# Performance work log

Measured on AMD Instinct MI355X. Metric: run time of the kernel, lower is better.

Reference implementation:

```python
import jax, jax.numpy as jnp
import numpy as np

DIM = 2048
D_INNER = 2048
B = 4
T = 4096
INIT_DECAY = 0.5


def setup_inputs() -> dict:
    key = jax.random.key(0)
    k1, k2, k3 = jax.random.split(key, 3)
    x = jax.random.normal(k1, (B, T, DIM), dtype=jnp.float32)
    h0 = jnp.zeros((B, D_INNER), dtype=jnp.float32)
    # xavier_uniform for Linear(dim -> d_inner) and Linear(d_inner -> dim)
    lim_in = float(np.sqrt(6.0 / (DIM + D_INNER)))
    W_in = jax.random.uniform(k2, (D_INNER, DIM), minval=-lim_in, maxval=lim_in, dtype=jnp.float32)
    lim_out = float(np.sqrt(6.0 / (D_INNER + DIM)))
    W_out = jax.random.uniform(k3, (DIM, D_INNER), minval=-lim_out, maxval=lim_out, dtype=jnp.float32)
    init_log = float(np.log(INIT_DECAY / (1.0 - INIT_DECAY)))  # logit(0.5) = 0
    log_d = jnp.full((D_INNER,), init_log, dtype=jnp.float32)
    b = jnp.zeros((D_INNER,), dtype=jnp.float32)
    return {"x": x, "h0": h0, "W_in": W_in, "W_out": W_out, "log_d": log_d, "b": b}


def reference(x, h0, W_in, W_out, log_d, b):
    # x: [B, T, dim]
    d = jax.nn.sigmoid(log_d)                       # [D] per-dim decay in (0,1)
    xp = jax.nn.silu(jnp.einsum('btd,ed->bte', x, W_in))  # [B, T, D_inner]
    xs = jnp.swapaxes(xp, 0, 1)                     # [T, B, D]

    def step(h_prev, xt):
        h_new = d * (xt + h_prev) + b               # diagonal-decay recurrence
        out = h_new * jax.nn.silu(h_new)            # self-gating
        return h_new, out

    h_final, outs = jax.lax.scan(step, h0, xs)      # outs: [T, B, D]
    cell_out = jnp.swapaxes(outs, 0, 1)             # [B, T, D]
    output = jnp.einsum('bte,de->btd', cell_out, W_out)  # [B, T, dim]
    return output, h_final
```

## Files before the change

### kernel.cpp

```cpp
#include <hip/hip_runtime.h>
#include <hip/hip_bf16.h>

#define DIMV 2048
#define DIV  2048
#define BV   4
#define TV   4096
#define MV   (BV * TV)
#define GK   2048
#define NCH  64
#define CH   64

typedef __bf16 bf16x8 __attribute__((ext_vector_type(8)));
typedef __bf16 bf16x4 __attribute__((ext_vector_type(4)));
typedef float  floatx4 __attribute__((ext_vector_type(4)));

__device__ __forceinline__ void gload_lds16(const void* g, void* l) {
    __builtin_amdgcn_global_load_lds((const __attribute__((address_space(1))) void*)g,
                                     (__attribute__((address_space(3))) void*)l,
                                     16, 0, 0);
}

__global__ __launch_bounds__(256) void cvt_all(const float4* __restrict__ x,
                                               const float4* __restrict__ wi,
                                               const float4* __restrict__ wo,
                                               ushort4* __restrict__ xb,
                                               ushort4* __restrict__ wib,
                                               ushort4* __restrict__ wob) {
    int i = blockIdx.x * 256 + threadIdx.x;
    const float4* src;
    ushort4* dst;
    int off;
    if (i < 8388608)       { src = x;  dst = xb;  off = 0; }
    else if (i < 9437184)  { src = wi; dst = wib; off = 8388608; }
    else                   { src = wo; dst = wob; off = 9437184; }
    float4 v = src[i - off];
    __hip_bfloat16 a = __float2bfloat16(v.x);
    __hip_bfloat16 b = __float2bfloat16(v.y);
    __hip_bfloat16 c = __float2bfloat16(v.z);
    __hip_bfloat16 d = __float2bfloat16(v.w);
    ushort4 o;
    o.x = *(unsigned short*)&a;
    o.y = *(unsigned short*)&b;
    o.z = *(unsigned short*)&c;
    o.w = *(unsigned short*)&d;
    dst[i - off] = o;
}

template <int EPI>
__global__ __launch_bounds__(512, 2) void gemm256_bt(const __hip_bfloat16* __restrict__ A,
                                                     const __hip_bfloat16* __restrict__ Bt,
                                                     float* __restrict__ Cf,
                                                     __hip_bfloat16* __restrict__ Cb) {
    __shared__ __align__(16) char AsB[65536];
    __shared__ __align__(16) char BsB[65536];

    const int tid  = threadIdx.x;
    const int lane = tid & 63;
    const int wave = tid >> 6;
    const int wmh  = wave >> 2;
    const int wnh  = (wave >> 1) & 1;
    const int wno  = wave & 1;
    const int lr   = lane & 15;
    const int lq   = lane >> 4;

    const int p   = blockIdx.y * gridDim.x + blockIdx.x;
    const int swz = (p & 7) * 64 + (p >> 3);
    const int m0  = (swz >> 3) * 256;
    const int n0  = (swz & 7) * 256;

    const int rdswz = lr * 128 + ((lq * 16) ^ ((lr & 7) << 4));
    const int rds[2] = { rdswz, rdswz ^ 64 };
    const char* aRd0 = AsB + wmh * 16384;
    const char* bRd0 = BsB + wnh * 16384 + wno * 8192;

    const int srow = tid >> 3;
    const int scol = ((tid & 7) ^ (srow & 7)) * 8;
    const __hip_bfloat16* aS_h0g0 = A  + (size_t)(m0 +   0 +  0 + srow) * GK + scol;
    const __hip_bfloat16* aS_h0g1 = A  + (size_t)(m0 +   0 + 64 + srow) * GK + scol;
    const __hip_bfloat16* aS_h1g0 = A  + (size_t)(m0 + 128 +  0 + srow) * GK + scol;
    const __hip_bfloat16* aS_h1g1 = A  + (size_t)(m0 + 128 + 64 + srow) * GK + scol;
    const __hip_bfloat16* bS_h0g0 = Bt + (size_t)(n0 +   0 +  0 + srow) * GK + scol;
    const __hip_bfloat16* bS_h0g1 = Bt + (size_t)(n0 +   0 + 64 + srow) * GK + scol;
    const __hip_bfloat16* bS_h1g0 = Bt + (size_t)(n0 + 128 +  0 + srow) * GK + scol;
    const __hip_bfloat16* bS_h1g1 = Bt + (size_t)(n0 + 128 + 64 + srow) * GK + scol;

#define BARR  asm volatile("s_barrier" ::: "memory")
#define WAITL do { asm volatile("s_waitcnt lgkmcnt(0)" ::: "memory");          \
                   __builtin_amdgcn_sched_barrier(0); } while (0)
#define VMW(N_) asm volatile("s_waitcnt vmcnt(" #N_ ")" ::: "memory")

#define STG(SRC_, DST_, T_) gload_lds16((SRC_) + (size_t)(T_) * 64, (DST_))
#define ST_AG0(T_, C_) do {                                                    \
    STG(aS_h0g0, AsB + (C_) * 32768 +     0 + tid * 16, T_);                   \
    STG(aS_h1g0, AsB + (C_) * 32768 + 16384 + tid * 16, T_); } while (0)
#define ST_AG1(T_, C_) do {                                                    \
    STG(aS_h0g1, AsB + (C_) * 32768 +  8192 + tid * 16, T_);                   \
    STG(aS_h1g1, AsB + (C_) * 32768 + 24576 + tid * 16, T_); } while (0)
#define ST_BG0(T_, C_) do {                                                    \
    STG(bS_h0g0, BsB + (C_) * 32768 +     0 + tid * 16, T_);                   \
    STG(bS_h1g0, BsB + (C_) * 32768 + 16384 + tid * 16, T_); } while (0)
#define ST_BG1(T_, C_) do {                                                    \
    STG(bS_h0g1, BsB + (C_) * 32768 +  8192 + tid * 16, T_);                   \
    STG(bS_h1g1, BsB + (C_) * 32768 + 24576 + tid * 16, T_); } while (0)

#define RDPH_A(DST_, MI0_, C_)                                                 \
    _Pragma("unroll") for (int mi_ = 0; mi_ < 4; ++mi_)                        \
      _Pragma("unroll") for (int s_ = 0; s_ < 2; ++s_)                         \
        DST_[mi_][s_] = *(const bf16x8*)(aRd0 + (C_) * 32768 +                 \
                                         ((MI0_) + mi_) * 2048 + rds[s_]);
#define RDPH_B(DST_, NI0_, C_)                                                 \
    _Pragma("unroll") for (int ni_ = 0; ni_ < 2; ++ni_)                        \
      _Pragma("unroll") for (int s_ = 0; s_ < 2; ++s_)                         \
        DST_[ni_][s_] = *(const bf16x8*)(bRd0 + (C_) * 32768 +                 \
                                         ((NI0_) + ni_) * 2048 + rds[s_]);

#define QUAD(MI0_, NI0_, AF_, BF_)                                             \
    __builtin_amdgcn_s_setprio(1);                                             \
    _Pragma("unroll") for (int mi_ = 0; mi_ < 4; ++mi_)                        \
      _Pragma("unroll") for (int ni_ = 0; ni_ < 2; ++ni_)                      \
        _Pragma("unroll") for (int s_ = 0; s_ < 2; ++s_)                       \
          acc[(MI0_) + mi_][(NI0_) + ni_] =                                    \
            __builtin_amdgcn_mfma_f32_16x16x32_bf16(                           \
              AF_[mi_][s_], BF_[ni_][s_],                                      \
              acc[(MI0_) + mi_][(NI0_) + ni_], 0, 0, 0);                       \
    __builtin_amdgcn_s_setprio(0);

#define KTILE(T_, C_, MODE_) do {                                              \
    bf16x8 a03[4][2], a47[4][2], b01[2][2], b23[2][2];                         \
                                                        \
    RDPH_A(a03, 0, C_);                                                        \
    RDPH_B(b01, 0, C_);                                                        \
    BARR; WAITL;                                                               \
    QUAD(0, 0, a03, b01);                                                      \
    BARR;                                                                      \
                                                        \
    RDPH_B(b23, 2, C_);                                                        \
    if ((MODE_) == 1) { ST_AG0((T_) + 2, C_); }                                \
    BARR; WAITL;                                                               \
    QUAD(0, 2, a03, b23);                                                      \
    BARR;                                                                      \
                                                        \
    RDPH_A(a47, 4, C_);                                                        \
    if ((MODE_) == 1) { ST_BG0((T_) + 2, C_); }                                \
    BARR; WAITL;                                                               \
    QUAD(4, 2, a47, b23);                                                      \
    BARR;                                                                      \
                                                        \
    if ((MODE_) == 1) { ST_AG1((T_) + 2, C_); ST_BG1((T_) + 2, C_); }          \
    BARR;                                                                      \
    QUAD(4, 0, a47, b01);                                                      \
    if ((MODE_) == 1) { VMW(8); }                                              \
    if ((MODE_) == 2) { VMW(0); }                                              \
    BARR;                                                                      \
} while (0)

    floatx4 acc[8][4];
#pragma unroll
    for (int i = 0; i < 8; ++i)
#pragma unroll
        for (int j = 0; j < 4; ++j) acc[i][j] = 0.f;

    ST_AG0(0, 0); ST_BG0(0, 0); ST_AG1(0, 0); ST_BG1(0, 0);
    ST_AG0(1, 1); ST_BG0(1, 1); ST_AG1(1, 1); ST_BG1(1, 1);
    VMW(8); BARR;

    for (int t2 = 0; t2 < 15; ++t2) {
        KTILE(2 * t2,     0, 1);
        KTILE(2 * t2 + 1, 1, 1);
    }
    KTILE(30, 0, 2);
    KTILE(31, 1, 0);

#undef KTILE
#undef QUAD
#undef RDPH_A
#undef RDPH_B
#undef ST_AG0
#undef ST_AG1
#undef ST_BG0
#undef ST_BG1
#undef STG
#undef VMW
#undef WAITL
#undef BARR

    const int wm = wmh * 128;
    const int wn = (wave & 3) * 64;
#pragma unroll
    for (int mi = 0; mi < 8; ++mi) {
#pragma unroll
        for (int r = 0; r < 4; ++r) {
            const int row = m0 + wm + mi * 16 + lq * 4 + r;
#pragma unroll
            for (int ni = 0; ni < 4; ++ni) {
                const int col = n0 + wn + ni * 16 + lr;
                float v = acc[mi][ni][r];
                if (EPI == 1) {
                    float s = v / (1.f + __expf(-v));
                    Cb[(size_t)row * DIV + col] = __float2bfloat16(s);
                } else {
                    Cf[(size_t)row * DIMV + col] = v;
                }
            }
        }
    }
}

__global__ __launch_bounds__(256) void scan_carry(const __hip_bfloat16* __restrict__ xp,
                                                  const float* __restrict__ logd,
                                                  const float* __restrict__ bias,
                                                  float* __restrict__ carry) {
    const int eg = blockIdx.x * 256 + threadIdx.x;
    const int e0 = eg * 4;
    const int c = blockIdx.y;
    const int b = blockIdx.z;
    const float4 ld = ((const float4*)logd)[eg];
    const float4 bb = ((const float4*)bias)[eg];
    float dv[4] = {1.f / (1.f + __expf(-ld.x)), 1.f / (1.f + __expf(-ld.y)),
                   1.f / (1.f + __expf(-ld.z)), 1.f / (1.f + __expf(-ld.w))};
    float bv[4] = {bb.x, bb.y, bb.z, bb.w};
    const __hip_bfloat16* p = xp + ((size_t)(b * TV + c * CH)) * DIV + e0;
    float h[4] = {0.f, 0.f, 0.f, 0.f};
#pragma unroll 8
    for (int i = 0; i < CH; ++i) {
        bf16x4 v = *(const bf16x4*)(p + (size_t)i * DIV);
#pragma unroll
        for (int j = 0; j < 4; ++j)
            h[j] = dv[j] * ((float)v[j] + h[j]) + bv[j];
    }
    float4 o = {h[0], h[1], h[2], h[3]};
    *(float4*)&carry[((size_t)b * NCH + c) * DIV + e0] = o;
}

__global__ __launch_bounds__(256) void scan_apply(const __hip_bfloat16* __restrict__ xp,
                                                  const float* __restrict__ logd,
                                                  const float* __restrict__ bias,
                                                  const float* __restrict__ h0,
                                                  const float* __restrict__ carry,
                                                  __hip_bfloat16* __restrict__ cell,
                                                  float* __restrict__ hfin) {
    const int eg = blockIdx.x * 256 + threadIdx.x;
    const int e0 = eg * 4;
    const int c = blockIdx.y;
    const int b = blockIdx.z;
    const float4 ld = ((const float4*)logd)[eg];
    const float4 bb = ((const float4*)bias)[eg];
    float dv[4] = {1.f / (1.f + __expf(-ld.x)), 1.f / (1.f + __expf(-ld.y)),
                   1.f / (1.f + __expf(-ld.z)), 1.f / (1.f + __expf(-ld.w))};
    float bv[4] = {bb.x, bb.y, bb.z, bb.w};
    float dCH[4];
#pragma unroll
    for (int j = 0; j < 4; ++j) dCH[j] = __powf(dv[j], (float)CH);

    float4 H4 = *(const float4*)&h0[(size_t)b * DIV + e0];
    float H[4] = {H4.x, H4.y, H4.z, H4.w};
    for (int j = 0; j < c; ++j) {
        float4 cr = *(const float4*)&carry[((size_t)b * NCH + j) * DIV + e0];
#pragma unroll
        for (int q = 0; q < 4; ++q) H[q] = dCH[q] * H[q] + ((const float*)&cr)[q];
    }

    const size_t base = ((size_t)(b * TV + c * CH)) * DIV + e0;
    float h[4] = {H[0], H[1], H[2], H[3]};
#pragma unroll 4
    for (int i = 0; i < CH; ++i) {
        bf16x4 v = *(const bf16x4*)(xp + base + (size_t)i * DIV);
        ushort4 o;
        unsigned short* op = (unsigned short*)&o;
#pragma unroll
        for (int j = 0; j < 4; ++j) {
            h[j] = dv[j] * ((float)v[j] + h[j]) + bv[j];
            float cv = h[j] * (h[j] / (1.f + __expf(-h[j])));
            __hip_bfloat16 cb = __float2bfloat16(cv);
            op[j] = *(unsigned short*)&cb;
        }
        *(ushort4*)(cell + base + (size_t)i * DIV) = o;
    }
    if (c == NCH - 1) {
        float4 o = {h[0], h[1], h[2], h[3]};
        *(float4*)&hfin[(size_t)b * DIV + e0] = o;
    }
}

extern "C" void kernel_launch(void* const* d_in, const int* in_sizes, int n_in,
                              void* d_out, int out_size, void* d_ws, size_t ws_size,
                              hipStream_t stream) {
    const float* x     = (const float*)d_in[0];
    const float* h0    = (const float*)d_in[1];
    const float* W_in  = (const float*)d_in[2];
    const float* W_out = (const float*)d_in[3];
    const float* log_d = (const float*)d_in[4];
    const float* bias  = (const float*)d_in[5];

    float* out  = (float*)d_out;
    float* hfin = out + (size_t)BV * TV * DIMV;

    char* ws = (char*)d_ws;
    __hip_bfloat16* xb    = (__hip_bfloat16*)ws;
    __hip_bfloat16* cellb = xb;
    __hip_bfloat16* wib   = (__hip_bfloat16*)(ws + 67108864);
    __hip_bfloat16* wob   = (__hip_bfloat16*)(ws + 67108864 + 8388608);
    __hip_bfloat16* xpb   = (__hip_bfloat16*)(ws + 67108864 + 16777216);
    float*          carry = (float*)(ws + 134217728 + 16777216);

    {
        int n4 = 10485760;
        cvt_all<<<n4 / 256, 256, 0, stream>>>((const float4*)x, (const float4*)W_in,
                                              (const float4*)W_out,
                                              (ushort4*)xb, (ushort4*)wib, (ushort4*)wob);
    }

    gemm256_bt<1><<<dim3(DIV / 256, MV / 256), 512, 0, stream>>>(xb, wib, nullptr, xpb);

    scan_carry<<<dim3(DIV / 1024, NCH, BV), 256, 0, stream>>>(xpb, log_d, bias, carry);
    scan_apply<<<dim3(DIV / 1024, NCH, BV), 256, 0, stream>>>(xpb, log_d, bias, h0, carry, cellb, hfin);

    gemm256_bt<0><<<dim3(DIMV / 256, MV / 256), 512, 0, stream>>>(cellb, wob, out, nullptr);
}
```

Baseline: 559.0 us.

## Prefetch next k-tile fragments across tiles and drop explicit LDS waits in GEMM

Restructures the GEMM k-tile loop so the A and B register fragments for the next k-tile are read from LDS during the current tile's last MFMA phases, double-buffering the b01 fragments across iterations. It removes the explicit lgkmcnt(0) waits and sched barriers, leaving the compiler to insert them, and reorders the global-to-LDS staging issues along with a new vmcnt wait point. This aims to hide LDS read latency behind MFMA work, at the cost of more live registers and tighter correctness reliance on the barrier and vmcnt placement.

Result: slower. 695.5 us (+24.4%).

```diff
diff --git a/kernel.cpp b/kernel.cpp
--- a/kernel.cpp
+++ b/kernel.cpp
@@ -85,8 +85,6 @@
     const __hip_bfloat16* bS_h1g1 = Bt + (size_t)(n0 + 128 + 64 + srow) * GK + scol;
 
 #define BARR  asm volatile("s_barrier" ::: "memory")
-#define WAITL do { asm volatile("s_waitcnt lgkmcnt(0)" ::: "memory");          \
-                   __builtin_amdgcn_sched_barrier(0); } while (0)
 #define VMW(N_) asm volatile("s_waitcnt vmcnt(" #N_ ")" ::: "memory")
 
 #define STG(SRC_, DST_, T_) gload_lds16((SRC_) + (size_t)(T_) * 64, (DST_))
@@ -125,32 +123,31 @@
               acc[(MI0_) + mi_][(NI0_) + ni_], 0, 0, 0);                       \
     __builtin_amdgcn_s_setprio(0);
 
-#define KTILE(T_, C_, MODE_) do {                                              \
-    bf16x8 a03[4][2], a47[4][2], b01[2][2], b23[2][2];                         \
-                                                        \
-    RDPH_A(a03, 0, C_);                                                        \
-    RDPH_B(b01, 0, C_);                                                        \
-    BARR; WAITL;                                                               \
-    QUAD(0, 0, a03, b01);                                                      \
-    BARR;                                                                      \
+#define KTILE(T_, C_, MODE_, B01C_, B01N_) do {                                \
                                                         \
     RDPH_B(b23, 2, C_);                                                        \
+    BARR;                                                                      \
+    QUAD(0, 0, a03, B01C_);                                                    \
+    BARR;                                                                      \
+                                                        \
     if ((MODE_) == 1) { ST_AG0((T_) + 2, C_); }                                \
-    BARR; WAITL;                                                               \
+    RDPH_A(a47, 4, C_);                                                        \
+    BARR;                                                                      \
     QUAD(0, 2, a03, b23);                                                      \
+    if ((MODE_) == 1) { VMW(2); }                                              \
+    if ((MODE_) == 2) { VMW(0); }                                              \
     BARR;                                                                      \
                                                         \
-    RDPH_A(a47, 4, C_);                                                        \
-    if ((MODE_) == 1) { ST_BG0((T_) + 2, C_); }                                \
-    BARR; WAITL;                                                               \
+    if ((MODE_) == 1) { ST_BG0((T_) + 2, C_); ST_BG1((T_) + 2, C_); }          \
+    if ((MODE_) != 3) { RDPH_A(a03, 0, (C_) ^ 1); }                            \
+    BARR;                                                                      \
     QUAD(4, 2, a47, b23);                                                      \
     BARR;                                                                      \
                                                         \
-    if ((MODE_) == 1) { ST_AG1((T_) + 2, C_); ST_BG1((T_) + 2, C_); }          \
-    BARR;                                                                      \
-    QUAD(4, 0, a47, b01);                                                      \
-    if ((MODE_) == 1) { VMW(8); }                                              \
-    if ((MODE_) == 2) { VMW(0); }                                              \
+    if ((MODE_) == 1) { ST_AG1((T_) + 2, C_); }                                \
+    if ((MODE_) != 3) { RDPH_B(B01N_, 0, (C_) ^ 1); }                          \
+    BARR;                                                                      \
+    QUAD(4, 0, a47, B01C_);                                                    \
     BARR;                                                                      \
 } while (0)
 
@@ -160,16 +157,20 @@
 #pragma unroll
         for (int j = 0; j < 4; ++j) acc[i][j] = 0.f;
 
-    ST_AG0(0, 0); ST_BG0(0, 0); ST_AG1(0, 0); ST_BG1(0, 0);
-    ST_AG0(1, 1); ST_BG0(1, 1); ST_AG1(1, 1); ST_BG1(1, 1);
+    bf16x8 a03[4][2], a47[4][2], b23[2][2], b01a[2][2], b01b[2][2];
+
+    ST_AG0(0, 0); ST_BG0(0, 0); ST_BG1(0, 0); ST_AG1(0, 0);
+    ST_AG0(1, 1); ST_BG0(1, 1); ST_BG1(1, 1); ST_AG1(1, 1);
     VMW(8); BARR;
+    RDPH_A(a03, 0, 0);
+    RDPH_B(b01a, 0, 0);
 
     for (int t2 = 0; t2 < 15; ++t2) {
-        KTILE(2 * t2,     0, 1);
-        KTILE(2 * t2 + 1, 1, 1);
-    }
-    KTILE(30, 0, 2);
-    KTILE(31, 1, 0);
+        KTILE(2 * t2,     0, 1, b01a, b01b);
+        KTILE(2 * t2 + 1, 1, 1, b01b, b01a);
+    }
+    KTILE(30, 0, 2, b01a, b01b);
+    KTILE(31, 1, 3, b01b, b01a);
 
 #undef KTILE
 #undef QUAD
@@ -181,7 +182,6 @@
 #undef ST_BG1
 #undef STG
 #undef VMW
-#undef WAITL
 #undef BARR
 
     const int wm = wmh * 128;
```
